# Kernel tuning notes

Measured on AMD Instinct MI355X. Metric: run time of the kernel, lower is better.

Reference implementation:

```python
import jax, jax.numpy as jnp
import numpy as np

B, HH, WW = 2, 64, 128
CX, CCONS = 117, 6
HEADS, HID = 4, 128
EDGE_DIM = 8
EMBED = 128
TGT = 39
E_EDGES = 131072
N_NODES = B * (HH * WW + 2)
LRELU = 0.01       # nn.LeakyReLU default
ATT_SLOPE = 0.2    # GATConv attention leaky slope
BN_EPS = 1e-5


def leaky(x, s=LRELU):
    return jnp.where(x >= 0, x, s * x)


def gat_conv(x, src, dst, edge_attr, W, att_src, att_dst, W_edge, att_edge, bias):
    """PyG GATConv (concat heads, add_self_loops=True, fill_value='mean')."""
    N = x.shape[0]
    E = src.shape[0]
    heads, C = att_src.shape
    # self-loop edge_attr = mean of incoming edge attrs (0 if none)
    cnt = jax.ops.segment_sum(jnp.ones((E,), x.dtype), dst, N)
    loop_attr = jax.ops.segment_sum(edge_attr, dst, N) / jnp.maximum(cnt, 1.0)[:, None]
    nodes = jnp.arange(N, dtype=src.dtype)
    s = jnp.concatenate([src, nodes])
    d = jnp.concatenate([dst, nodes])
    ea = jnp.concatenate([edge_attr, loop_attr], axis=0)
    xp = (x @ W).reshape(N, heads, C)                    # [N,h,c]
    a_src = (xp * att_src).sum(-1)                       # [N,h]
    a_dst = (xp * att_dst).sum(-1)
    ep = (ea @ W_edge).reshape(-1, heads, C)             # [E+N,h,c]
    a_edge = (ep * att_edge).sum(-1)
    alpha = leaky(a_src[s] + a_dst[d] + a_edge, ATT_SLOPE)   # [E+N,h]
    amax = jax.ops.segment_max(alpha, d, N)
    ex = jnp.exp(alpha - amax[d])
    w = ex / jax.ops.segment_sum(ex, d, N)[d]
    msg = xp[s] * w[:, :, None]                          # [E+N,h,c]
    out = jax.ops.segment_sum(msg, d, N).reshape(N, heads * C)
    return out + bias


def local_map(x):
    """Periodic longitude pad + pole rows (rolled by W/2), as construct_local_map."""
    b, c, h, w = x.shape
    mid = jnp.concatenate([x[..., -1:], x, x[..., :1]], axis=-1)            # [b,c,h,w+2]
    top = jnp.concatenate([x[:, :, 1, w // 2 - 1:], x[:, :, 1, :w // 2 + 1]], axis=-1)[:, :, None, :]
    bot = jnp.concatenate([x[:, :, -2, w // 2 - 1:], x[:, :, -2, :w // 2 + 1]], axis=-1)[:, :, None, :]
    return jnp.concatenate([top, mid, bot], axis=2)                          # [b,c,h+2,w+2]


def setup_inputs() -> dict:
    key = jax.random.key(0)
    ks = jax.random.split(key, 32)
    def nrm(i, shape, scale=0.1):
        return jax.random.normal(ks[i], shape, jnp.float32) * scale
    x = nrm(0, (B, CX, HH, WW), 1.0)
    x_cons = nrm(1, (B, CCONS, HH, WW), 1.0)
    src = jax.random.randint(ks[2], (E_EDGES,), 0, N_NODES)
    off = jax.random.randint(ks[3], (E_EDGES,), 1, N_NODES)
    dst = (src + off) % N_NODES                       # guarantees no self-loops
    edge_index = jnp.stack([src, dst]).astype(jnp.int32)
    edge_attr = nrm(4, (E_EDGES, EDGE_DIM), 1.0)
    F1 = CX + CCONS
    HC = HEADS * HID
    params = dict(
        g1_W=nrm(5, (F1, HC)), g1_as=nrm(6, (HEADS, HID)), g1_ad=nrm(7, (HEADS, HID)),
        g1_We=nrm(8, (EDGE_DIM, HC)), g1_ae=nrm(9, (HEADS, HID)), g1_b=nrm(10, (HC,)),
        g2_W=nrm(11, (HC, HC)), g2_as=nrm(12, (HEADS, HID)), g2_ad=nrm(13, (HEADS, HID)),
        g2_We=nrm(14, (EDGE_DIM, HC)), g2_ae=nrm(15, (HEADS, HID)), g2_b=nrm(16, (HC,)),
        conv_w=nrm(17, (EMBED, HC, 3, 3), 0.02), conv_b=nrm(18, (EMBED,)),
        bn_g=jnp.ones((EMBED,), jnp.float32), bn_b=jnp.zeros((EMBED,), jnp.float32),
        m_w1=nrm(19, (HC + EMBED, 512), 0.05), m_b1=nrm(20, (512,)),
        m_w2=nrm(21, (512, 256), 0.05), m_b2=nrm(22, (256,)),
        m_w3=nrm(23, (256, TGT), 0.05), m_b3=nrm(24, (TGT,)),
    )
    return dict(x=x, x_cons=x_cons, edge_index=edge_index, edge_attr=edge_attr, **params)


def _forward(x, x_cons, edge_index, edge_attr,
             g1_W, g1_as, g1_ad, g1_We, g1_ae, g1_b,
             g2_W, g2_as, g2_ad, g2_We, g2_ae, g2_b,
             conv_w, conv_b, bn_g, bn_b,
             m_w1, m_b1, m_w2, m_b2, m_w3, m_b3):
    src, dst = edge_index[0], edge_index[1]
    feats = jnp.concatenate([x, x_cons], axis=1)                 # [B,123,H,W]
    nodes = jnp.transpose(feats, (0, 2, 3, 1)).reshape(B, HH * WW, -1)
    poles = jnp.zeros((B, 2, nodes.shape[-1]), nodes.dtype)
    nodes = jnp.concatenate([poles, nodes], axis=1).reshape(B * (HH * WW + 2), -1)
    h = leaky(gat_conv(nodes, src, dst, edge_attr, g1_W, g1_as, g1_ad, g1_We, g1_ae, g1_b))
    h = leaky(gat_conv(h, src, dst, edge_attr, g2_W, g2_as, g2_ad, g2_We, g2_ae, g2_b))
    g = h.reshape(B, HH * WW + 2, -1)[:, 2:, :]                  # drop pole nodes
    gm = jnp.transpose(g.reshape(B, HH, WW, -1), (0, 3, 1, 2))   # [B,512,H,W]
    lm = local_map(gm)                                           # [B,512,H+2,W+2]
    conv = jax.lax.conv_general_dilated(lm, conv_w, (1, 1), 'VALID',
                                        dimension_numbers=('NCHW', 'OIHW', 'NCHW'))
    conv = conv + conv_b[None, :, None, None]
    # BatchNorm2d in eval mode (running_mean=0, running_var=1)
    bn = conv * (bn_g / jnp.sqrt(1.0 + BN_EPS))[None, :, None, None] + bn_b[None, :, None, None]
    nl = leaky(bn)
    nl_flat = jnp.transpose(nl, (0, 2, 3, 1)).reshape(-1, EMBED)
    xf = g.reshape(-1, HEADS * HID)
    z = jnp.concatenate([xf, nl_flat], axis=-1)                  # [B*H*W, 640]
    z = leaky(z @ m_w1 + m_b1)
    z = leaky(z @ m_w2 + m_b2)
    z = z @ m_w3 + m_b3
    delta = jnp.transpose(z.reshape(B, HH, WW, TGT), (0, 3, 1, 2))
    return delta + x[:, -TGT:]


def reference(x, x_cons, edge_index, edge_attr,
              g1_W, g1_as, g1_ad, g1_We, g1_ae, g1_b,
              g2_W, g2_as, g2_ad, g2_We, g2_ae, g2_b,
              conv_w, conv_b, bn_g, bn_b,
              m_w1, m_b1, m_w2, m_b2, m_w3, m_b3):
    return _forward(x, x_cons, edge_index, edge_attr,
                    g1_W, g1_as, g1_ad, g1_We, g1_ae, g1_b,
                    g2_W, g2_as, g2_ad, g2_We, g2_ae, g2_b,
                    conv_w, conv_b, bn_g, bn_b,
                    m_w1, m_b1, m_w2, m_b2, m_w3, m_b3)
```

## Files before the change

### kernel.cpp

```cpp
#include <hip/hip_runtime.h>
#include <math.h>
#include <type_traits>

#define NB    2
#define HHH   64
#define WWW   128
#define F1    123
#define HC    512
#define NE    131072
#define PB    8194
#define NNODE (NB*PB)
#define NPOS  (NB*HHH*WWW)
#define TGT   39
#define EMBED 128
#define KCONV 4608
#define NTAPK 1152

static inline int ceildiv(int a, int b){ return (a + b - 1) / b; }

typedef short v8s __attribute__((ext_vector_type(8)));
typedef short v4s __attribute__((ext_vector_type(4)));
typedef float v4f __attribute__((ext_vector_type(4)));

__device__ __forceinline__ float leakyf(float x, float s){ return x >= 0.f ? x : s * x; }

__device__ __forceinline__ unsigned short f2b(float f) {
  unsigned u = __builtin_bit_cast(unsigned, f);
  u = (u + 0x7FFFu + ((u >> 16) & 1u)) >> 16;
  return (unsigned short)u;
}
__device__ __forceinline__ float b2f(unsigned short h) {
  unsigned u = ((unsigned)h) << 16;
  return __builtin_bit_cast(float, u);
}

__device__ __forceinline__ void gload_lds16(const void* g, void* l) {
  __builtin_amdgcn_global_load_lds((const __attribute__((address_space(1))) void*)g,
                                   (__attribute__((address_space(3))) void*)l, 16, 0, 0);
}

__global__ __launch_bounds__(256) void k_build_nodes(const float* __restrict__ x,
                                                     const float* __restrict__ xc,
                                                     unsigned short* __restrict__ nodes) {
  __shared__ unsigned short lds[64][130];
  int blk = blockIdx.x;
  int b = blk >> 7, p0 = (blk & 127) * 64;
  int tid = threadIdx.x;
  int pi = tid & 63, cg = tid >> 6;
  for (int c = cg; c < 128; c += 4) {
    float v = 0.f;
    int p = p0 + pi;
    if (c < 117)      v = x[((size_t)(b * 117 + c)) * 8192 + p];
    else if (c < 123) v = xc[((size_t)(b * 6 + (c - 117))) * 8192 + p];
    lds[pi][c] = f2b(v);
  }
  if ((blk & 127) == 0 && tid < 32) {
    int rr = tid >> 4, sg = tid & 15;
    *(v8s*)(nodes + ((size_t)(b * PB + rr)) * 128 + sg * 8) = (v8s)0;
  }
  __syncthreads();
  int seg = tid & 15, r0 = tid >> 4;
  for (int rr = r0; rr < 64; rr += 16) {
    int node = b * PB + 2 + p0 + rr;
    *(v8s*)(nodes + (size_t)node * 128 + seg * 8) = *(const v8s*)(&lds[rr][seg * 8]);
  }
}

__global__ void k_hist(const int* __restrict__ dst, int* __restrict__ cnt) {
  int e = blockIdx.x * blockDim.x + threadIdx.x;
  if (e >= NE) return;
  atomicAdd(&cnt[dst[e]], 1);
}

__global__ void k_scan(const int* __restrict__ cnt, int* __restrict__ rowptr,
                       int* __restrict__ cursor, int n) {
  __shared__ int part[512];
  int t = threadIdx.x;
  int chunk = (n + 511) >> 9;
  int beg = t * chunk, end = min(beg + chunk, n);
  int s = 0;
  for (int i = beg; i < end; i++) s += cnt[i];
  part[t] = s;
  __syncthreads();
  int own = s;
  for (int off = 1; off < 512; off <<= 1) {
    int v = 0;
    if (t >= off) v = part[t - off];
    __syncthreads();
    part[t] += v;
    __syncthreads();
  }
  int run = part[t] - own;
  for (int i = beg; i < end; i++) { rowptr[i] = run; cursor[i] = run; run += cnt[i]; }
  if (t == 511) rowptr[n] = part[511];
}

__global__ void k_scatter(const int* __restrict__ dst, int* __restrict__ cursor,
                          int* __restrict__ colidx) {
  int e = blockIdx.x * blockDim.x + threadIdx.x;
  if (e >= NE) return;
  int pos = atomicAdd(&cursor[dst[e]], 1);
  colidx[pos] = e;
}

__global__ void k_loop_attr(const float* __restrict__ eattr, const int* __restrict__ rowptr,
                            const int* __restrict__ colidx, float* __restrict__ lattr) {
  int idx = blockIdx.x * blockDim.x + threadIdx.x;
  if (idx >= NNODE * 8) return;
  int nn = idx >> 3, k = idx & 7;
  int b = rowptr[nn], e = rowptr[nn + 1];
  float s = 0.f;
  for (int i = b; i < e; i++) s += eattr[(size_t)colidx[i] * 8 + k];
  int c = e - b;
  lattr[idx] = s / (float)max(c, 1);
}

__global__ void k_prep(const float* __restrict__ g1W, const float* __restrict__ g2W,
                       const float* __restrict__ convw, const float* __restrict__ mw1,
                       const float* __restrict__ mw2, const float* __restrict__ mw3,
                       unsigned short* __restrict__ g1Wt, unsigned short* __restrict__ g2Wt,
                       unsigned short* __restrict__ convWt, unsigned short* __restrict__ mw1t,
                       unsigned short* __restrict__ mw2t, unsigned short* __restrict__ mw3t) {
  int idx = blockIdx.x * blockDim.x + threadIdx.x;
  if (idx < 65536) {
    int n = idx >> 7, k = idx & 127;
    g1Wt[idx] = (k < F1) ? f2b(g1W[(size_t)k * 512 + n]) : (unsigned short)0;
  } else if ((idx -= 65536) < 262144) {
    int n = idx >> 9, k = idx & 511;
    g2Wt[idx] = f2b(g2W[(size_t)k * 512 + n]);
  } else if ((idx -= 262144) < 589824) {
    int j = idx >> 9, c = idx & 511;
    int tap = j >> 7, nn = j & 127;
    convWt[idx] = f2b(convw[(size_t)nn * KCONV + c * 9 + tap]);
  } else if ((idx -= 589824) < 327680) {
    int n = idx / 640, k = idx - n * 640;
    mw1t[idx] = f2b(mw1[(size_t)k * 512 + n]);
  } else if ((idx -= 327680) < 131072) {
    int n = idx >> 9, k = idx & 511;
    mw2t[idx] = f2b(mw2[(size_t)k * 256 + n]);
  } else if ((idx -= 131072) < 9984) {
    int n = idx >> 8, k = idx & 255;
    mw3t[idx] = f2b(mw3[(size_t)k * TGT + n]);
  }
}

__global__ void k_medge2(const float* __restrict__ We1, const float* __restrict__ ae1,
                         const float* __restrict__ We2, const float* __restrict__ ae2,
                         float* __restrict__ M2) {
  int t = threadIdx.x;
  if (t >= 32) return;
  const float* We = blockIdx.x ? We2 : We1;
  const float* ae = blockIdx.x ? ae2 : ae1;
  int k = t >> 2, h = t & 3;
  float s = 0.f;
  for (int c = 0; c < 128; c++) s += We[k * 512 + h * 128 + c] * ae[h * 128 + c];
  M2[blockIdx.x * 32 + t] = s;
}

__global__ void k_aedge2(const float* __restrict__ eattr, const float* __restrict__ lattr,
                         const float* __restrict__ M2,
                         float* __restrict__ ae1, float* __restrict__ ae2,
                         float* __restrict__ al1, float* __restrict__ al2) {
  int idx = blockIdx.x * blockDim.x + threadIdx.x;
  if (idx >= (NE + NNODE) * 4) return;
  int e = idx >> 2, h = idx & 3;
  const float* src;
  float *o1, *o2;
  if (e < NE) { src = eattr + (size_t)e * 8; o1 = ae1 + idx; o2 = ae2 + idx; }
  else {
    int n = e - NE;
    src = lattr + (size_t)n * 8;
    o1 = al1 + n * 4 + h; o2 = al2 + n * 4 + h;
  }
  float s1 = 0.f, s2 = 0.f;
#pragma unroll
  for (int k = 0; k < 8; k++) {
    float a = src[k];
    s1 += a * M2[k * 4 + h];
    s2 += a * M2[32 + k * 4 + h];
  }
  *o1 = s1; *o2 = s2;
}

__global__ void k_attn_dots(const unsigned short* __restrict__ xp, const float* __restrict__ as,
                            const float* __restrict__ ad, float* __restrict__ a_src,
                            float* __restrict__ a_dst) {
  int gw = (blockIdx.x * blockDim.x + threadIdx.x) >> 6;
  int lane = threadIdx.x & 63;
  if (gw >= NNODE) return;
  int h = lane >> 4;
  int c0 = (lane & 15) * 8;
  v8s v = *(const v8s*)(xp + (size_t)gw * HC + h * 128 + c0);
  const float* asr = as + h * 128 + c0;
  const float* adr = ad + h * 128 + c0;
  float s1 = 0.f, s2 = 0.f;
#pragma unroll
  for (int i = 0; i < 8; i++) {
    float f = b2f((unsigned short)v[i]);
    s1 += f * asr[i]; s2 += f * adr[i];
  }
  for (int off = 1; off < 16; off <<= 1) { s1 += __shfl_xor(s1, off); s2 += __shfl_xor(s2, off); }
  if ((lane & 15) == 0) { a_src[gw * 4 + h] = s1; a_dst[gw * 4 + h] = s2; }
}

__global__ __launch_bounds__(256) void k_aggregate(
    const unsigned short* __restrict__ xp, const float* __restrict__ a_src,
    const float* __restrict__ a_dst, const float* __restrict__ a_edge,
    const float* __restrict__ a_eloop, const int* __restrict__ srcv,
    const int* __restrict__ rowptr, const int* __restrict__ colidx,
    const float* __restrict__ bias, unsigned short* __restrict__ outp,
    int ldo, int pole) {
  int wid = threadIdx.x >> 6, lane = threadIdx.x & 63;
  int n = blockIdx.x * 4 + wid;
  if (n >= NNODE) return;
  if (pole) {
    int b = n / PB, loc = n - b * PB;
    if (loc < 2) return;
    outp += (size_t)(b * 8192 + loc - 2) * ldo;
  } else {
    outp += (size_t)n * ldo;
  }
  int beg = rowptr[n], deg = rowptr[n + 1] - beg;
  int total = deg + 1;
  int ha = lane & 3;
  int ea = lane >> 2;
  int hh = lane >> 4;
  int c0 = lane * 8;
  float adn = a_dst[(size_t)n * 4 + ha];
  float m0 = -1e30f, m1 = -1e30f, m2 = -1e30f, m3 = -1e30f;
  float l0 = 0.f, l1 = 0.f, l2 = 0.f, l3 = 0.f;
  float acc[8] = {0.f, 0.f, 0.f, 0.f, 0.f, 0.f, 0.f, 0.f};
  for (int base = 0; base < total; base += 16) {
    int cnt = min(16, total - base);
    int ge = base + ea;
    int sn = n;
    float al = -1e30f;
    if (ea < cnt) {
      float aev;
      if (ge < deg) { int eid = colidx[beg + ge]; sn = srcv[eid]; aev = a_edge[(size_t)eid * 4 + ha]; }
      else          { aev = a_eloop[(size_t)n * 4 + ha]; }
      al = leakyf(a_src[(size_t)sn * 4 + ha] + adn + aev, 0.2f);
    }
    float cm = al;
    cm = fmaxf(cm, __shfl_xor(cm, 4));
    cm = fmaxf(cm, __shfl_xor(cm, 8));
    cm = fmaxf(cm, __shfl_xor(cm, 16));
    cm = fmaxf(cm, __shfl_xor(cm, 32));
    float cm0 = __shfl(cm, 0), cm1 = __shfl(cm, 1), cm2 = __shfl(cm, 2), cm3 = __shfl(cm, 3);
    float nm0 = fmaxf(m0, cm0), nm1 = fmaxf(m1, cm1), nm2 = fmaxf(m2, cm2), nm3 = fmaxf(m3, cm3);
    float r0 = __expf(m0 - nm0), r1 = __expf(m1 - nm1), r2 = __expf(m2 - nm2), r3 = __expf(m3 - nm3);
    float nmh = ha == 0 ? nm0 : ha == 1 ? nm1 : ha == 2 ? nm2 : nm3;
    float ex = (ea < cnt) ? __expf(al - nmh) : 0.f;
    float s = ex;
    s += __shfl_xor(s, 4);
    s += __shfl_xor(s, 8);
    s += __shfl_xor(s, 16);
    s += __shfl_xor(s, 32);
    float s0 = __shfl(s, 0), s1 = __shfl(s, 1), s2 = __shfl(s, 2), s3 = __shfl(s, 3);
    l0 = l0 * r0 + s0; l1 = l1 * r1 + s1; l2 = l2 * r2 + s2; l3 = l3 * r3 + s3;
    m0 = nm0; m1 = nm1; m2 = nm2; m3 = nm3;
    float rh = hh == 0 ? r0 : hh == 1 ? r1 : hh == 2 ? r2 : r3;
#pragma unroll
    for (int j = 0; j < 8; j++) acc[j] *= rh;
    for (int e0 = 0; e0 < cnt; e0 += 4) {
      int nb = min(4, cnt - e0);
      v8s vv[4]; float wt[4];
#pragma unroll
      for (int u = 0; u < 4; u++) {
        if (u < nb) {
          int e = e0 + u;
          wt[u] = __shfl(ex, e * 4 + hh);
          int se = __shfl(sn, e * 4);
          vv[u] = *(const v8s*)(xp + (size_t)se * HC + c0);
        }
      }
#pragma unroll
      for (int u = 0; u < 4; u++) {
        if (u < nb) {
#pragma unroll
          for (int j = 0; j < 8; j++) acc[j] += wt[u] * b2f((unsigned short)vv[u][j]);
        }
      }
    }
  }
  float lh = hh == 0 ? l0 : hh == 1 ? l1 : hh == 2 ? l2 : l3;
  float inv = 1.f / lh;
  v8s o;
#pragma unroll
  for (int j = 0; j < 8; j++) {
    float v = acc[j] * inv + bias[c0 + j];
    o[j] = (short)f2b(leakyf(v, 0.01f));
  }
  *(v8s*)(outp + c0) = o;
}

template<int BM, int BN, typename OutT>
__global__ __launch_bounds__(256) void mgemm(
    int M, int N, int K, int ldb,
    const unsigned short* __restrict__ A, int lda,
    const unsigned short* __restrict__ Bt,
    const float* __restrict__ bias,
    float slope,
    OutT* __restrict__ C, int ldc)
{
  constexpr int WM = BM / 32;
  constexpr int WN = BN / 32;
  constexpr int NA = BM * 4 / 256;
  constexpr int NBC = BN * 4 / 256;
  constexpr int STAGE_USH = 2 * (BM + BN) * 32;
  constexpr int REPACK_USH = 32 * BN * 2;
  constexpr int SMEM_USH = STAGE_USH > REPACK_USH ? STAGE_USH : REPACK_USH;
  __shared__ unsigned short smem[SMEM_USH];
  int tid = threadIdx.x;
  int wid = tid >> 6, lane = tid & 63;
  int wr = wid >> 1, wc = wid & 1;
  int l15 = lane & 15, l4 = lane >> 4;

  int gx = gridDim.x;
  int nwg = gx * gridDim.y;
  int slot = blockIdx.x + blockIdx.y * gx;
  int qv = nwg >> 3, rv = nwg & 7;
  int xcd = slot & 7, pos = slot >> 3;
  int wg = (xcd < rv ? xcd * (qv + 1) : rv * (qv + 1) + (xcd - rv) * qv) + pos;
  int bx = wg % gx, by = wg / gx;
  int row0 = by * BM, col0 = bx * BN;

  const unsigned short* pa[NA];
  const unsigned short* pb[NBC];
#pragma unroll
  for (int i = 0; i < NA; i++) {
    int c = i * 256 + tid, r2 = c >> 2, seg = c & 3;
    pa[i] = A + (size_t)min(row0 + r2, M - 1) * lda + seg * 8;
  }
#pragma unroll
  for (int i = 0; i < NBC; i++) {
    int c = i * 256 + tid, r2 = c >> 2, seg = c & 3;
    pb[i] = Bt + (size_t)min(col0 + r2, N - 1) * ldb + seg * 8;
  }

  auto stage = [&](int buf, int kt) {
    int k0 = kt * 32;
    unsigned short* as = smem + buf * (BM * 32);
    unsigned short* bs = smem + 2 * BM * 32 + buf * (BN * 32);
#pragma unroll
    for (int i = 0; i < NA; i++)
      gload_lds16(pa[i] + k0, as + (i * 256 + tid) * 8);
#pragma unroll
    for (int i = 0; i < NBC; i++)
      gload_lds16(pb[i] + k0, bs + (i * 256 + tid) * 8);
  };

  v4f acc[WM][WN];
#pragma unroll
  for (int m = 0; m < WM; m++)
#pragma unroll
    for (int n = 0; n < WN; n++) acc[m][n] = (v4f)0.f;

  int nt = K >> 5;
  stage(0, 0);
  __syncthreads();
  int cur = 0;
  for (int t = 0; t < nt - 1; t++) {
    stage(cur ^ 1, t + 1);
    const unsigned short* as = smem + cur * (BM * 32);
    const unsigned short* bs = smem + 2 * BM * 32 + cur * (BN * 32);
    v8s a[WM], b[WN];
#pragma unroll
    for (int m = 0; m < WM; m++)
      a[m] = *(const v8s*)(as + (wr * (BM / 2) + m * 16 + l15) * 32 + l4 * 8);
#pragma unroll
    for (int n = 0; n < WN; n++)
      b[n] = *(const v8s*)(bs + (wc * (BN / 2) + n * 16 + l15) * 32 + l4 * 8);
#pragma unroll
    for (int m = 0; m < WM; m++)
#pragma unroll
      for (int n = 0; n < WN; n++)
        acc[m][n] = __builtin_amdgcn_mfma_f32_16x16x32_bf16(a[m], b[n], acc[m][n], 0, 0, 0);
    __syncthreads();
    cur ^= 1;
  }
  {
    const unsigned short* as = smem + cur * (BM * 32);
    const unsigned short* bs = smem + 2 * BM * 32 + cur * (BN * 32);
    v8s a[WM], b[WN];
#pragma unroll
    for (int m = 0; m < WM; m++)
      a[m] = *(const v8s*)(as + (wr * (BM / 2) + m * 16 + l15) * 32 + l4 * 8);
#pragma unroll
    for (int n = 0; n < WN; n++)
      b[n] = *(const v8s*)(bs + (wc * (BN / 2) + n * 16 + l15) * 32 + l4 * 8);
#pragma unroll
    for (int m = 0; m < WM; m++)
#pragma unroll
      for (int n = 0; n < WN; n++)
        acc[m][n] = __builtin_amdgcn_mfma_f32_16x16x32_bf16(a[m], b[n], acc[m][n], 0, 0, 0);
  }

  if constexpr (std::is_same<OutT, float>::value) {
#pragma unroll
    for (int m = 0; m < WM; m++) {
#pragma unroll
      for (int q2 = 0; q2 < 4; q2++) {
        int r2 = row0 + wr * (BM / 2) + m * 16 + l4 * 4 + q2;
        if (r2 >= M) continue;
#pragma unroll
        for (int n = 0; n < WN; n++) {
          int cc = col0 + wc * (BN / 2) + n * 16 + l15;
          if (cc >= N) continue;
          float v = acc[m][n][q2];
          if (bias) v += bias[cc];
          v = leakyf(v, slope);
          C[(size_t)r2 * ldc + cc] = v;
        }
      }
    }
  } else {
    __syncthreads();
    float* rb = (float*)smem;
    for (int m = 0; m < WM; m++) {
#pragma unroll
      for (int n = 0; n < WN; n++)
#pragma unroll
        for (int q2 = 0; q2 < 4; q2++)
          rb[(wr * 16 + l4 * 4 + q2) * BN + wc * (BN / 2) + n * 16 + l15] = acc[m][n][q2];
      __syncthreads();
#pragma unroll
      for (int it = 0; it < (32 * BN) / 1024; it++) {
        int f = it * 1024 + tid * 4;
        int lr = f / BN, lc = f % BN;
        int rr = row0 + (lr >> 4) * (BM / 2) + m * 16 + (lr & 15);
        if (rr < M) {
          v4f vv = *(const v4f*)(rb + lr * BN + lc);
          v4s o;
#pragma unroll
          for (int j = 0; j < 4; j++) {
            float v = vv[j];
            if (bias) v += bias[col0 + lc + j];
            v = leakyf(v, slope);
            o[j] = (short)f2b(v);
          }
          *(v4s*)(C + (size_t)rr * ldc + col0 + lc) = o;
        }
      }
      __syncthreads();
    }
  }
}

__global__ void k_tapsum(const unsigned short* __restrict__ H,
                         const float* __restrict__ convb, const float* __restrict__ bng,
                         const float* __restrict__ bnb, unsigned short* __restrict__ zin) {
  int idx = blockIdx.x * blockDim.x + threadIdx.x;
  if (idx >= NPOS * 16) return;
  int r = idx >> 4, seg = idx & 15;
  int n0 = seg * 8;
  int b = r >> 13, pos = r & 8191, i = pos >> 7, j = pos & 127;
  float acc[8] = {0.f, 0.f, 0.f, 0.f, 0.f, 0.f, 0.f, 0.f};
#pragma unroll
  for (int tap = 0; tap < 9; tap++) {
    int di = tap / 3, dj = tap - di * 3;
    int rr = i + di, cc = j + dj;
    int gr, gc;
    if (rr == 0)       { gr = 1;      gc = (63 + cc) & 127; }
    else if (rr == 65) { gr = 62;     gc = (63 + cc) & 127; }
    else               { gr = rr - 1; gc = (cc + 127) & 127; }
    v8s v = *(const v8s*)(H + ((size_t)(b * 8192 + gr * WWW + gc)) * NTAPK + tap * 128 + n0);
#pragma unroll
    for (int q = 0; q < 8; q++) acc[q] += b2f((unsigned short)v[q]);
  }
  unsigned short* o = zin + (size_t)r * 640 + 512 + n0;
  v8s ov;
#pragma unroll
  for (int q = 0; q < 8; q++) {
    int cc = n0 + q;
    float v = acc[q] + convb[cc];
    v = v * (bng[cc] * rsqrtf(1.f + 1e-5f)) + bnb[cc];
    ov[q] = (short)f2b(leakyf(v, 0.01f));
  }
  *(v8s*)o = ov;
}

__global__ void k_final(const float* __restrict__ z3, const float* __restrict__ x,
                        float* __restrict__ outp) {
  int idx = blockIdx.x * blockDim.x + threadIdx.x;
  if (idx >= NPOS * TGT) return;
  int b = idx / (TGT * 8192);
  int rem = idx - b * (TGT * 8192);
  int t = rem >> 13;
  int p = rem & 8191;
  outp[idx] = z3[((size_t)(b * 8192 + p)) * TGT + t] + x[((size_t)(b * 117 + 78 + t)) * 8192 + p];
}

extern "C" void kernel_launch(void* const* d_in, const int* in_sizes, int n_in,
                              void* d_out, int out_size, void* d_ws, size_t ws_size,
                              hipStream_t stream) {
  const float* x     = (const float*)d_in[0];
  const float* xcons = (const float*)d_in[1];
  const int*   eidx  = (const int*)d_in[2];
  const float* eattr = (const float*)d_in[3];
  const float* g1W  = (const float*)d_in[4];
  const float* g1as = (const float*)d_in[5];
  const float* g1ad = (const float*)d_in[6];
  const float* g1We = (const float*)d_in[7];
  const float* g1ae = (const float*)d_in[8];
  const float* g1b  = (const float*)d_in[9];
  const float* g2W  = (const float*)d_in[10];
  const float* g2as = (const float*)d_in[11];
  const float* g2ad = (const float*)d_in[12];
  const float* g2We = (const float*)d_in[13];
  const float* g2ae = (const float*)d_in[14];
  const float* g2b  = (const float*)d_in[15];
  const float* convw= (const float*)d_in[16];
  const float* convb= (const float*)d_in[17];
  const float* bng  = (const float*)d_in[18];
  const float* bnb  = (const float*)d_in[19];
  const float* mw1  = (const float*)d_in[20];
  const float* mb1  = (const float*)d_in[21];
  const float* mw2  = (const float*)d_in[22];
  const float* mb2  = (const float*)d_in[23];
  const float* mw3  = (const float*)d_in[24];
  const float* mb3  = (const float*)d_in[25];
  float* outp = (float*)d_out;
  (void)in_sizes; (void)n_in; (void)out_size; (void)ws_size;

  const int* esrc = eidx;
  const int* edst = eidx + NE;

  char* basep = (char*)d_ws;
  size_t off = 0;
  auto alloc = [&](size_t bytes) -> void* {
    void* p = basep + off;
    off += (bytes + 255) & ~(size_t)255;
    return p;
  };
  unsigned short* nodesb = (unsigned short*)alloc((size_t)NNODE * 128 * 2);
  unsigned short* xpb    = (unsigned short*)alloc((size_t)NNODE * HC * 2);
  unsigned short* h1b    = (unsigned short*)alloc((size_t)NNODE * HC * 2);
  unsigned short* zin    = (unsigned short*)alloc((size_t)NPOS * 640 * 2);
  unsigned short* Hb     = (unsigned short*)alloc((size_t)NPOS * NTAPK * 2);
  float* asrc   = (float*)alloc((size_t)NNODE * 4 * sizeof(float));
  float* adst   = (float*)alloc((size_t)NNODE * 4 * sizeof(float));
  float* aedge1 = (float*)alloc((size_t)NE * 4 * sizeof(float));
  float* aedge2 = (float*)alloc((size_t)NE * 4 * sizeof(float));
  float* aeloop1= (float*)alloc((size_t)NNODE * 4 * sizeof(float));
  float* aeloop2= (float*)alloc((size_t)NNODE * 4 * sizeof(float));
  float* lattr  = (float*)alloc((size_t)NNODE * 8 * sizeof(float));
  float* M2     = (float*)alloc(64 * sizeof(float));
  unsigned short* g1Wt  = (unsigned short*)alloc((size_t)512 * 128 * 2);
  unsigned short* g2Wt  = (unsigned short*)alloc((size_t)512 * 512 * 2);
  unsigned short* convWt= (unsigned short*)alloc((size_t)NTAPK * 512 * 2);
  unsigned short* mw1t  = (unsigned short*)alloc((size_t)512 * 640 * 2);
  unsigned short* mw2t  = (unsigned short*)alloc((size_t)256 * 512 * 2);
  unsigned short* mw3t  = (unsigned short*)alloc((size_t)TGT * 256 * 2);
  int* cnt      = (int*)alloc((size_t)NNODE * sizeof(int));
  int* rowptr   = (int*)alloc((size_t)(NNODE + 1) * sizeof(int));
  int* cursor   = (int*)alloc((size_t)NNODE * sizeof(int));
  int* colidx   = (int*)alloc((size_t)NE * sizeof(int));
  unsigned short* z1b = xpb;
  unsigned short* z2b = h1b;
  float*          z3  = (float*)nodesb;

  hipMemsetAsync(cnt, 0, NNODE * sizeof(int), stream);
  k_build_nodes<<<NB * 128, 256, 0, stream>>>(x, xcons, nodesb);
  k_hist<<<ceildiv(NE, 256), 256, 0, stream>>>(edst, cnt);
  k_scan<<<1, 512, 0, stream>>>(cnt, rowptr, cursor, NNODE);
  k_scatter<<<ceildiv(NE, 256), 256, 0, stream>>>(edst, cursor, colidx);
  k_loop_attr<<<ceildiv(NNODE * 8, 256), 256, 0, stream>>>(eattr, rowptr, colidx, lattr);

  k_prep<<<ceildiv(1386240, 256), 256, 0, stream>>>(g1W, g2W, convw, mw1, mw2, mw3,
                                                    g1Wt, g2Wt, convWt, mw1t, mw2t, mw3t);
  k_medge2<<<2, 64, 0, stream>>>(g1We, g1ae, g2We, g2ae, M2);
  k_aedge2<<<ceildiv((NE + NNODE) * 4, 256), 256, 0, stream>>>(
      eattr, lattr, M2, aedge1, aedge2, aeloop1, aeloop2);

  {
    dim3 g(4, ceildiv(NNODE, 128));
    mgemm<128, 128, unsigned short><<<g, 256, 0, stream>>>(
        NNODE, HC, 128, 128, nodesb, 128, g1Wt, nullptr, 1.0f, xpb, HC);
  }
  k_attn_dots<<<ceildiv(NNODE, 4), 256, 0, stream>>>(xpb, g1as, g1ad, asrc, adst);
  k_aggregate<<<ceildiv(NNODE, 4), 256, 0, stream>>>(xpb, asrc, adst, aedge1, aeloop1, esrc,
                                                     rowptr, colidx, g1b, h1b, HC, 0);

  {
    dim3 g(4, ceildiv(NNODE, 128));
    mgemm<128, 128, unsigned short><<<g, 256, 0, stream>>>(
        NNODE, HC, HC, HC, h1b, HC, g2Wt, nullptr, 1.0f, xpb, HC);
  }
  k_attn_dots<<<ceildiv(NNODE, 4), 256, 0, stream>>>(xpb, g2as, g2ad, asrc, adst);
  k_aggregate<<<ceildiv(NNODE, 4), 256, 0, stream>>>(xpb, asrc, adst, aedge2, aeloop2, esrc,
                                                     rowptr, colidx, g2b, zin, 640, 1);

  {
    dim3 g(NTAPK / 128, ceildiv(NPOS, 128));
    mgemm<128, 128, unsigned short><<<g, 256, 0, stream>>>(
        NPOS, NTAPK, 512, 512, zin, 640, convWt, nullptr, 1.0f, Hb, NTAPK);
  }
  k_tapsum<<<ceildiv(NPOS * 16, 256), 256, 0, stream>>>(Hb, convb, bng, bnb, zin);

  {
    dim3 g(4, ceildiv(NPOS, 128));
    mgemm<128, 128, unsigned short><<<g, 256, 0, stream>>>(
        NPOS, 512, 640, 640, zin, 640, mw1t, mb1, 0.01f, z1b, 512);
  }
  {
    dim3 g(2, ceildiv(NPOS, 64));
    mgemm<64, 128, unsigned short><<<g, 256, 0, stream>>>(
        NPOS, 256, 512, 512, z1b, 512, mw2t, mb2, 0.01f, z2b, 256);
  }
  {
    dim3 g(1, ceildiv(NPOS, 64));
    mgemm<64, 64, float><<<g, 256, 0, stream>>>(
        NPOS, TGT, 256, 256, z2b, 256, mw3t, mb3, 1.0f, z3, TGT);
  }

  k_final<<<ceildiv(NPOS * TGT, 256), 256, 0, stream>>>(z3, x, outp);
}
```

Before: 304.3 us.

## Replace tap-expanded conv GEMM with implicit-GEMM split over kernel rows

The 3x3 conv used to run as a GEMM producing 9 tap outputs per position (N=1152), which were written to a large bf16 buffer and then gathered and summed by a separate kernel. It is now an implicit GEMM that gathers shifted neighbour rows of the input straight into shared memory and accumulates over channels times taps (K=4608). The work is split into 3 chunks, one per kernel row, whose fp32 partial sums are added by a small reduce kernel that also applies bias, batchnorm and leaky ReLU. This removes the bf16 rounding of each tap product and the 9x-wide intermediate buffer. In exchange it writes three fp32 partial buffers, uses a smaller 64x128 tile with simple double buffering, and adds an XCD-aware block remap.

```diff
diff --git a/kernel.cpp b/kernel.cpp
--- a/kernel.cpp
+++ b/kernel.cpp
@@ -14,7 +14,7 @@
 #define TGT   39
 #define EMBED 128
 #define KCONV 4608
-#define NTAPK 1152
+#define CSPLIT 3
 
 static inline int ceildiv(int a, int b){ return (a + b - 1) / b; }
 
@@ -129,9 +129,10 @@
     int n = idx >> 9, k = idx & 511;
     g2Wt[idx] = f2b(g2W[(size_t)k * 512 + n]);
   } else if ((idx -= 262144) < 589824) {
-    int j = idx >> 9, c = idx & 511;
-    int tap = j >> 7, nn = j & 127;
-    convWt[idx] = f2b(convw[(size_t)nn * KCONV + c * 9 + tap]);
+    int j = idx >> 9;
+    int n = j / 9, tap = j - n * 9;
+    int c = idx & 511;
+    convWt[idx] = f2b(convw[(size_t)n * KCONV + c * 9 + tap]);
   } else if ((idx -= 589824) < 327680) {
     int n = idx / 640, k = idx - n * 640;
     mw1t[idx] = f2b(mw1[(size_t)k * 512 + n]);
@@ -447,37 +448,141 @@
   }
 }
 
-__global__ void k_tapsum(const unsigned short* __restrict__ H,
-                         const float* __restrict__ convb, const float* __restrict__ bng,
-                         const float* __restrict__ bnb, unsigned short* __restrict__ zin) {
+__global__ __launch_bounds__(256) void cgemm(
+    const unsigned short* __restrict__ zin,
+    const unsigned short* __restrict__ Wt,
+    float* __restrict__ C)
+{
+  constexpr int BM = 64, BN = 128, WM = 2, WN = 4;
+  __shared__ unsigned short smem[2 * (BM + BN) * 32];
+  int tid = threadIdx.x;
+  int wid = tid >> 6, lane = tid & 63;
+  int wr = wid >> 1, wc = wid & 1;
+  int l15 = lane & 15, l4 = lane >> 4;
+
+  int gx = gridDim.x;
+  int nwg = gx * gridDim.y;
+  int slot = blockIdx.x + blockIdx.y * gx;
+  int qv = nwg >> 3, rv = nwg & 7;
+  int xcd = slot & 7, pos = slot >> 3;
+  int wg = (xcd < rv ? xcd * (qv + 1) : rv * (qv + 1) + (xcd - rv) * qv) + pos;
+  int chunk = wg % gx, by = wg / gx;
+  int row0 = by * BM;
+
+  int r2 = tid >> 2, seg = tid & 3;
+  int p = row0 + r2;
+  int b = p >> 13, pos2 = p & 8191, ii = pos2 >> 7, jj = pos2 & 127;
+  int rr = ii + chunk;
+  auto mk = [&](int dj) -> const unsigned short* {
+    int cc2 = jj + dj;
+    int gr, gc;
+    if (rr == 0)       { gr = 1;      gc = (63 + cc2) & 127; }
+    else if (rr == 65) { gr = 62;     gc = (63 + cc2) & 127; }
+    else               { gr = rr - 1; gc = (cc2 + 127) & 127; }
+    return zin + ((size_t)(b * 8192 + gr * WWW + gc)) * 640 + seg * 8;
+  };
+  const unsigned short* pa0 = mk(0);
+  const unsigned short* pa1 = mk(1);
+  const unsigned short* pa2 = mk(2);
+  const unsigned short* pb0;
+  const unsigned short* pb1;
+  {
+    int c = tid, rb2 = c >> 2, sb = c & 3;
+    pb0 = Wt + (size_t)rb2 * KCONV + chunk * 1536 + sb * 8;
+    c = 256 + tid; rb2 = c >> 2; sb = c & 3;
+    pb1 = Wt + (size_t)rb2 * KCONV + chunk * 1536 + sb * 8;
+  }
+
+  auto stage = [&](int buf, int kt) {
+    int k0 = kt * 32;
+    int tl = k0 >> 9, coff = k0 & 511;
+    const unsigned short* pA = tl == 0 ? pa0 : (tl == 1 ? pa1 : pa2);
+    unsigned short* as = smem + buf * (BM * 32);
+    unsigned short* bs = smem + 2 * BM * 32 + buf * (BN * 32);
+    gload_lds16(pA + coff, as + tid * 8);
+    gload_lds16(pb0 + k0, bs + tid * 8);
+    gload_lds16(pb1 + k0, bs + (256 + tid) * 8);
+  };
+
+  v4f acc[WM][WN];
+#pragma unroll
+  for (int m = 0; m < WM; m++)
+#pragma unroll
+    for (int n = 0; n < WN; n++) acc[m][n] = (v4f)0.f;
+
+  constexpr int nt = 48;
+  stage(0, 0);
+  __syncthreads();
+  int cur = 0;
+  for (int t = 0; t < nt - 1; t++) {
+    stage(cur ^ 1, t + 1);
+    const unsigned short* as = smem + cur * (BM * 32);
+    const unsigned short* bs = smem + 2 * BM * 32 + cur * (BN * 32);
+    v8s a[WM], b[WN];
+#pragma unroll
+    for (int m = 0; m < WM; m++)
+      a[m] = *(const v8s*)(as + (wr * 32 + m * 16 + l15) * 32 + l4 * 8);
+#pragma unroll
+    for (int n = 0; n < WN; n++)
+      b[n] = *(const v8s*)(bs + (wc * 64 + n * 16 + l15) * 32 + l4 * 8);
+#pragma unroll
+    for (int m = 0; m < WM; m++)
+#pragma unroll
+      for (int n = 0; n < WN; n++)
+        acc[m][n] = __builtin_amdgcn_mfma_f32_16x16x32_bf16(a[m], b[n], acc[m][n], 0, 0, 0);
+    __syncthreads();
+    cur ^= 1;
+  }
+  {
+    const unsigned short* as = smem + cur * (BM * 32);
+    const unsigned short* bs = smem + 2 * BM * 32 + cur * (BN * 32);
+    v8s a[WM], b[WN];
+#pragma unroll
+    for (int m = 0; m < WM; m++)
+      a[m] = *(const v8s*)(as + (wr * 32 + m * 16 + l15) * 32 + l4 * 8);
+#pragma unroll
+    for (int n = 0; n < WN; n++)
+      b[n] = *(const v8s*)(bs + (wc * 64 + n * 16 + l15) * 32 + l4 * 8);
+#pragma unroll
+    for (int m = 0; m < WM; m++)
+#pragma unroll
+      for (int n = 0; n < WN; n++)
+        acc[m][n] = __builtin_amdgcn_mfma_f32_16x16x32_bf16(a[m], b[n], acc[m][n], 0, 0, 0);
+  }
+  float* Cc = C + (size_t)chunk * NPOS * 128;
+#pragma unroll
+  for (int m = 0; m < WM; m++) {
+#pragma unroll
+    for (int q2 = 0; q2 < 4; q2++) {
+      int rw = row0 + wr * 32 + m * 16 + l4 * 4 + q2;
+#pragma unroll
+      for (int n = 0; n < WN; n++) {
+        int cc = wc * 64 + n * 16 + l15;
+        Cc[(size_t)rw * 128 + cc] = acc[m][n][q2];
+      }
+    }
+  }
+}
+
+__global__ void k_creduce(const float* __restrict__ p, const float* __restrict__ convb,
+                          const float* __restrict__ bng, const float* __restrict__ bnb,
+                          unsigned short* __restrict__ zin) {
   int idx = blockIdx.x * blockDim.x + threadIdx.x;
-  if (idx >= NPOS * 16) return;
-  int r = idx >> 4, seg = idx & 15;
-  int n0 = seg * 8;
-  int b = r >> 13, pos = r & 8191, i = pos >> 7, j = pos & 127;
-  float acc[8] = {0.f, 0.f, 0.f, 0.f, 0.f, 0.f, 0.f, 0.f};
-#pragma unroll
-  for (int tap = 0; tap < 9; tap++) {
-    int di = tap / 3, dj = tap - di * 3;
-    int rr = i + di, cc = j + dj;
-    int gr, gc;
-    if (rr == 0)       { gr = 1;      gc = (63 + cc) & 127; }
-    else if (rr == 65) { gr = 62;     gc = (63 + cc) & 127; }
-    else               { gr = rr - 1; gc = (cc + 127) & 127; }
-    v8s v = *(const v8s*)(H + ((size_t)(b * 8192 + gr * WWW + gc)) * NTAPK + tap * 128 + n0);
-#pragma unroll
-    for (int q = 0; q < 8; q++) acc[q] += b2f((unsigned short)v[q]);
-  }
-  unsigned short* o = zin + (size_t)r * 640 + 512 + n0;
-  v8s ov;
-#pragma unroll
-  for (int q = 0; q < 8; q++) {
-    int cc = n0 + q;
-    float v = acc[q] + convb[cc];
+  if (idx >= NPOS * 32) return;
+  int r = idx >> 5, c4 = (idx & 31) * 4;
+  const float4* p0 = (const float4*)(p + (size_t)r * 128 + c4);
+  const float4* p1 = (const float4*)(p + (size_t)(NPOS + r) * 128 + c4);
+  const float4* p2 = (const float4*)(p + (size_t)(2 * NPOS + r) * 128 + c4);
+  float4 a = *p0, b = *p1, c = *p2;
+  unsigned short* o = zin + (size_t)r * 640 + 512 + c4;
+#pragma unroll
+  for (int j = 0; j < 4; j++) {
+    float v = ((const float*)&a)[j] + ((const float*)&b)[j] + ((const float*)&c)[j];
+    int cc = c4 + j;
+    v += convb[cc];
     v = v * (bng[cc] * rsqrtf(1.f + 1e-5f)) + bnb[cc];
-    ov[q] = (short)f2b(leakyf(v, 0.01f));
-  }
-  *(v8s*)o = ov;
+    o[j] = f2b(leakyf(v, 0.01f));
+  }
 }
 
 __global__ void k_final(const float* __restrict__ z3, const float* __restrict__ x,
@@ -537,7 +642,7 @@
   unsigned short* xpb    = (unsigned short*)alloc((size_t)NNODE * HC * 2);
   unsigned short* h1b    = (unsigned short*)alloc((size_t)NNODE * HC * 2);
   unsigned short* zin    = (unsigned short*)alloc((size_t)NPOS * 640 * 2);
-  unsigned short* Hb     = (unsigned short*)alloc((size_t)NPOS * NTAPK * 2);
+  float* cpart  = (float*)alloc((size_t)CSPLIT * NPOS * 128 * sizeof(float));
   float* asrc   = (float*)alloc((size_t)NNODE * 4 * sizeof(float));
   float* adst   = (float*)alloc((size_t)NNODE * 4 * sizeof(float));
   float* aedge1 = (float*)alloc((size_t)NE * 4 * sizeof(float));
@@ -548,7 +653,7 @@
   float* M2     = (float*)alloc(64 * sizeof(float));
   unsigned short* g1Wt  = (unsigned short*)alloc((size_t)512 * 128 * 2);
   unsigned short* g2Wt  = (unsigned short*)alloc((size_t)512 * 512 * 2);
-  unsigned short* convWt= (unsigned short*)alloc((size_t)NTAPK * 512 * 2);
+  unsigned short* convWt= (unsigned short*)alloc((size_t)EMBED * KCONV * 2);
   unsigned short* mw1t  = (unsigned short*)alloc((size_t)512 * 640 * 2);
   unsigned short* mw2t  = (unsigned short*)alloc((size_t)256 * 512 * 2);
   unsigned short* mw3t  = (unsigned short*)alloc((size_t)TGT * 256 * 2);
@@ -592,11 +697,10 @@
                                                      rowptr, colidx, g2b, zin, 640, 1);
 
   {
-    dim3 g(NTAPK / 128, ceildiv(NPOS, 128));
-    mgemm<128, 128, unsigned short><<<g, 256, 0, stream>>>(
-        NPOS, NTAPK, 512, 512, zin, 640, convWt, nullptr, 1.0f, Hb, NTAPK);
-  }
-  k_tapsum<<<ceildiv(NPOS * 16, 256), 256, 0, stream>>>(Hb, convb, bng, bnb, zin);
+    dim3 g(CSPLIT, NPOS / 64);
+    cgemm<<<g, 256, 0, stream>>>(zin, convWt, cpart);
+  }
+  k_creduce<<<ceildiv(NPOS * 32, 256), 256, 0, stream>>>(cpart, convb, bng, bnb, zin);
 
   {
     dim3 g(4, ceildiv(NPOS, 128));
```

Result: no change. 303.6 us, median of 2 (-0.2%).
